# Kernel tuning notes

Measured on AMD Instinct MI355X. Metric: run time of the kernel, lower is better.

## Reference

```python
import jax, jax.numpy as jnp
import numpy as np

H = 8          # num heads
LN_EPS = 1e-5  # torch LayerNorm default

_SHAPES = {
    'src': (1024, 8, 256), 'pos': (1024, 8, 256), 'query_embed': (80, 8, 256), 'cam_mask': (8, 80, 1024),
    'enc_qkv_w': (2, 768, 256), 'enc_qkv_b': (2, 768), 'enc_out_w': (2, 256, 256), 'enc_out_b': (2, 256),
    'enc_ln1_g': (2, 256), 'enc_ln1_b': (2, 256),
    'enc_ff1_w': (2, 2048, 256), 'enc_ff1_b': (2, 2048), 'enc_ff2_w': (2, 256, 2048), 'enc_ff2_b': (2, 256),
    'enc_ln2_g': (2, 256), 'enc_ln2_b': (2, 256),
    'dec_sa_qkv_w': (2, 768, 256), 'dec_sa_qkv_b': (2, 768), 'dec_sa_out_w': (2, 256, 256), 'dec_sa_out_b': (2, 256),
    'dec_ln1_g': (2, 256), 'dec_ln1_b': (2, 256),
    'dec_ca_qkv_w': (2, 768, 256), 'dec_ca_qkv_b': (2, 768), 'dec_ca_out_w': (2, 256, 256), 'dec_ca_out_b': (2, 256),
    'dec_ln2_g': (2, 256), 'dec_ln2_b': (2, 256),
    'dec_ff1_w': (2, 2048, 256), 'dec_ff1_b': (2, 2048), 'dec_ff2_w': (2, 256, 2048), 'dec_ff2_b': (2, 256),
    'dec_ln3_g': (2, 256), 'dec_ln3_b': (2, 256),
    'dec_norm_g': (256,), 'dec_norm_b': (256,),
}


def setup_inputs() -> dict:
    key = jax.random.key(0)
    out = {}
    for i, (name, sh) in enumerate(_SHAPES.items()):
        k = jax.random.fold_in(key, i)
        if name.endswith('_g'):
            out[name] = jnp.ones(sh, jnp.float32)
        elif name.endswith('ln1_b') or name.endswith('ln2_b') or name.endswith('ln3_b') or name == 'dec_norm_b':
            out[name] = jnp.zeros(sh, jnp.float32)
        else:
            scale = 1.0 if name in ('src', 'pos', 'query_embed', 'cam_mask') else 0.02
            out[name] = jax.random.normal(k, sh, dtype=jnp.float32) * scale
    return out


def layer_norm(x, g, b):
    mu = jnp.mean(x, axis=-1, keepdims=True)
    var = jnp.mean(jnp.square(x - mu), axis=-1, keepdims=True)
    return (x - mu) * jax.lax.rsqrt(var + LN_EPS) * g + b


def mha(q_in, k_in, v_in, qkv_w, qkv_b, out_w, out_b, bias=None):
    # q_in: [L,B,D], k_in/v_in: [S,B,D]; torch layout: projections are x @ W.T + b
    L, B, D = q_in.shape
    S = k_in.shape[0]
    hd = D // H
    wq, wk, wv = qkv_w[:D], qkv_w[D:2 * D], qkv_w[2 * D:]
    bq, bk, bv = qkv_b[:D], qkv_b[D:2 * D], qkv_b[2 * D:]
    q = (q_in @ wq.T + bq).reshape(L, B, H, hd).transpose(1, 2, 0, 3)  # [B,H,L,hd]
    k = (k_in @ wk.T + bk).reshape(S, B, H, hd).transpose(1, 2, 0, 3)  # [B,H,S,hd]
    v = (v_in @ wv.T + bv).reshape(S, B, H, hd).transpose(1, 2, 0, 3)
    logits = jnp.einsum('bhld,bhsd->bhls', q, k) * (1.0 / np.sqrt(hd))
    if bias is not None:
        logits = logits + bias[:, None, :, :]  # CAM bias broadcast over heads
    attn = jax.nn.softmax(logits, axis=-1)
    o = jnp.einsum('bhls,bhsd->bhld', attn, v).transpose(2, 0, 1, 3).reshape(L, B, D)
    return o @ out_w.T + out_b


def reference(src, pos, query_embed, cam_mask,
              enc_qkv_w, enc_qkv_b, enc_out_w, enc_out_b, enc_ln1_g, enc_ln1_b,
              enc_ff1_w, enc_ff1_b, enc_ff2_w, enc_ff2_b, enc_ln2_g, enc_ln2_b,
              dec_sa_qkv_w, dec_sa_qkv_b, dec_sa_out_w, dec_sa_out_b, dec_ln1_g, dec_ln1_b,
              dec_ca_qkv_w, dec_ca_qkv_b, dec_ca_out_w, dec_ca_out_b, dec_ln2_g, dec_ln2_b,
              dec_ff1_w, dec_ff1_b, dec_ff2_w, dec_ff2_b, dec_ln3_g, dec_ln3_b,
              dec_norm_g, dec_norm_b):
    n_enc = enc_qkv_w.shape[0]
    n_dec = dec_sa_qkv_w.shape[0]
    # --- encoder (post-norm DETR style, pos added to q,k) ---
    mem = src
    for i in range(n_enc):
        qk = mem + pos
        a = mha(qk, qk, mem, enc_qkv_w[i], enc_qkv_b[i], enc_out_w[i], enc_out_b[i])
        mem = layer_norm(mem + a, enc_ln1_g[i], enc_ln1_b[i])
        f = jax.nn.relu(mem @ enc_ff1_w[i].T + enc_ff1_b[i]) @ enc_ff2_w[i].T + enc_ff2_b[i]
        mem = layer_norm(mem + f, enc_ln2_g[i], enc_ln2_b[i])
    # --- decoder: tgt starts at zeros (Q2L), query_embed is query_pos ---
    tgt = jnp.zeros_like(query_embed)
    for i in range(n_dec):
        qk = tgt + query_embed
        sa = mha(qk, qk, tgt, dec_sa_qkv_w[i], dec_sa_qkv_b[i], dec_sa_out_w[i], dec_sa_out_b[i])
        tgt = layer_norm(tgt + sa, dec_ln1_g[i], dec_ln1_b[i])
        ca = mha(tgt + query_embed, mem + pos, mem,
                 dec_ca_qkv_w[i], dec_ca_qkv_b[i], dec_ca_out_w[i], dec_ca_out_b[i],
                 bias=cam_mask)  # MA: CAM-derived additive attention bias [B,L,S]
        tgt = layer_norm(tgt + ca, dec_ln2_g[i], dec_ln2_b[i])
        f = jax.nn.relu(tgt @ dec_ff1_w[i].T + dec_ff1_b[i]) @ dec_ff2_w[i].T + dec_ff2_b[i]
        tgt = layer_norm(tgt + f, dec_ln3_g[i], dec_ln3_b[i])
    out = layer_norm(tgt, dec_norm_g, dec_norm_b)
    return out[None]  # [1, L, B, D] as in TransformerDecoder's output.unsqueeze(0)
```

## Files before the change

kernel.cpp:

```cpp
#include <hip/hip_runtime.h>
#include <hip/hip_bf16.h>
#include <cstdint>
#include <cstddef>

typedef __hip_bfloat16 bf16;
typedef float f4 __attribute__((ext_vector_type(4)));
typedef float f32x4 __attribute__((ext_vector_type(4)));
typedef short s8v __attribute__((ext_vector_type(8)));
typedef unsigned short u16x4 __attribute__((ext_vector_type(4)));
typedef unsigned short u16x8 __attribute__((ext_vector_type(8)));

#define LN_EPS 1e-5f
#define LOG2E 1.4426950408889634f

#if __has_builtin(__builtin_amdgcn_exp2f)
__device__ __forceinline__ float EXP2(float x) { return __builtin_amdgcn_exp2f(x); }
#else
__device__ __forceinline__ float EXP2(float x) {
  float r; asm("v_exp_f32 %0, %1" : "=v"(r) : "v"(x)); return r;
}
#endif

__device__ __forceinline__ void async_cp16(const void* g, void* lds) {
  __builtin_amdgcn_global_load_lds(
      (const __attribute__((address_space(1))) unsigned int*)g,
      (__attribute__((address_space(3))) unsigned int*)lds, 16, 0, 0);
}

__device__ __forceinline__ uint32_t pkbf(float lo, float hi) {
#if __has_builtin(__builtin_amdgcn_perm)
  uint32_t l = __builtin_bit_cast(uint32_t, lo) + 0x8000u;
  uint32_t h = __builtin_bit_cast(uint32_t, hi) + 0x8000u;
  return __builtin_amdgcn_perm(h, l, 0x07060302u);
#else
  uint32_t l = __builtin_bit_cast(uint32_t, lo) + 0x8000u;
  uint32_t h = __builtin_bit_cast(uint32_t, hi) + 0x8000u;
  return (l >> 16) | (h & 0xFFFF0000u);
#endif
}

#define NCAST 17
struct CastArgs {
  const float* in[NCAST];
  bf16* out[NCAST];
  int end4[NCAST];
  int nseg;
};

__global__ __launch_bounds__(256) void cast_multi(CastArgs a, int total4) {
  int i = blockIdx.x * 256 + threadIdx.x;
  if (i >= total4) return;
  int s = 0;
  while (i >= a.end4[s]) ++s;
  int j = i - (s ? a.end4[s - 1] : 0);
  f4 v = ((const f4*)a.in[s])[j];
  u16x4 o;
#pragma unroll
  for (int c = 0; c < 4; ++c) {
    bf16 h = __float2bfloat16(v[c]);
    o[c] = *reinterpret_cast<unsigned short*>(&h);
  }
  ((u16x4*)a.out[s])[j] = o;
}

__global__ __launch_bounds__(256) void scale_f32_kernel(const float* __restrict__ in,
                                                        float* __restrict__ out,
                                                        float s, int n4) {
  int i = blockIdx.x * 256 + threadIdx.x;
  if (i < n4) {
    f4 v = ((const f4*)in)[i];
    ((f4*)out)[i] = v * s;
  }
}

__global__ __launch_bounds__(256) void add_bf16_kernel(const float* __restrict__ a,
                                                       const float* __restrict__ b,
                                                       bf16* __restrict__ out, int n4) {
  int i = blockIdx.x * 256 + threadIdx.x;
  if (i < n4) {
    f4 x = ((const f4*)a)[i];
    f4 y = ((const f4*)b)[i];
    u16x4 o;
#pragma unroll
    for (int j = 0; j < 4; ++j) {
      bf16 h = __float2bfloat16(x[j] + y[j]);
      o[j] = *reinterpret_cast<unsigned short*>(&h);
    }
    ((u16x4*)out)[i] = o;
  }
}

__global__ __launch_bounds__(256) void sa0_row(
    const float* __restrict__ Wo, const float* __restrict__ bv,
    const float* __restrict__ bo, const float* __restrict__ g,
    const float* __restrict__ b, float* __restrict__ row_out) {
  const int j = threadIdx.x;
  float acc = bo[j];
  for (int k = 0; k < 256; k += 4) {
    f4 w = *(const f4*)(Wo + (size_t)j * 256 + k);
    f4 v = *(const f4*)(bv + k);
    acc += w[0] * v[0] + w[1] * v[1] + w[2] * v[2] + w[3] * v[3];
  }
  float s = acc, s2 = acc * acc;
#pragma unroll
  for (int off = 32; off >= 1; off >>= 1) {
    s += __shfl_down(s, off);
    s2 += __shfl_down(s2, off);
  }
  __shared__ float red[8];
  int wv = j >> 6;
  if ((j & 63) == 0) { red[wv] = s; red[4 + wv] = s2; }
  __syncthreads();
  if (j == 0) {
    float ts = red[0] + red[1] + red[2] + red[3];
    float ts2 = red[4] + red[5] + red[6] + red[7];
    float mu = ts * (1.f / 256.f);
    float var = ts2 * (1.f / 256.f) - mu * mu;
    red[0] = mu;
    red[1] = rsqrtf(var + LN_EPS);
  }
  __syncthreads();
  row_out[j] = (acc - red[0]) * red[1] * g[j] + b[j];
}

__global__ __launch_bounds__(256) void sa0_bcast(
    const float* __restrict__ row, const float* __restrict__ qe,
    float* __restrict__ tgt, bf16* __restrict__ tgtb, bf16* __restrict__ tqkb) {
  const int r = blockIdx.x, j = threadIdx.x;
  float y = row[j];
  size_t idx = (size_t)r * 256 + j;
  tgt[idx] = y;
  tgtb[idx] = __float2bfloat16(y);
  tqkb[idx] = __float2bfloat16(y + qe[idx]);
}

template <int TB, int MODE, int SPLITK>
__global__ __launch_bounds__(256, 2) void mfma_gemm(
    const bf16* __restrict__ A, const bf16* __restrict__ W,
    const float* __restrict__ bias, float* __restrict__ C,
    bf16* __restrict__ Cb, int M, int N, int K, int HL, float qscale,
    const bf16* __restrict__ A2, bf16* __restrict__ Cb2, int nyA, int secV) {
  constexpr int WM = TB / 2, WN = TB / 2;
  constexpr int MR = WM / 16, NR = WN / 16;
  constexpr int NCH = TB / 32;
  __shared__ __attribute__((aligned(16))) unsigned short SH[TB * 128];
  unsigned short (*As)[64] = (unsigned short(*)[64])SH;
  unsigned short (*Ws)[64] = (unsigned short(*)[64])(SH + TB * 64);
  const int tid = threadIdx.x;
  const int lane = tid & 63, wave = tid >> 6;
  const int wr = wave >> 1, wc = wave & 1;
  const int bm = blockIdx.x * TB, bn = blockIdx.y * TB;
  const int fr = lane & 15, fo = lane >> 4;
  const int srowi = lane >> 3;
  const int slot = lane & 7;
  const int gcol = (slot ^ srowi) * 8;

  const bf16* Aeff = (MODE == 6) ? (((int)blockIdx.y < nyA) ? A : A2) : A;

  const int kchunk = K / SPLITK;
  const int kbeg = (SPLITK > 1) ? blockIdx.z * kchunk : 0;

  f32x4 acc[MR][NR] = {};

  for (int k0 = kbeg; k0 < kbeg + kchunk; k0 += 64) {
    __syncthreads();
#pragma unroll
    for (int c = 0; c < NCH; ++c) {
      int rbase = wave * (TB / 4) + c * 8;
      int row = rbase + srowi;
      async_cp16(Aeff + (size_t)(bm + row) * K + k0 + gcol, &As[rbase][0]);
      async_cp16(W + (size_t)(bn + row) * K + k0 + gcol, &Ws[rbase][0]);
    }
    __syncthreads();
#pragma unroll
    for (int ks = 0; ks < 2; ++ks) {
      s8v a[MR], b[NR];
#pragma unroll
      for (int mi = 0; mi < MR; ++mi) {
        int row = wr * WM + mi * 16 + fr;
        a[mi] = *(const s8v*)((const char*)&As[0][0] + row * 128 +
                              ((ks * 64 + fo * 16) ^ ((row & 7) << 4)));
      }
#pragma unroll
      for (int ni = 0; ni < NR; ++ni) {
        int row = wc * WN + ni * 16 + fr;
        b[ni] = *(const s8v*)((const char*)&Ws[0][0] + row * 128 +
                              ((ks * 64 + fo * 16) ^ ((row & 7) << 4)));
      }
#pragma unroll
      for (int mi = 0; mi < MR; ++mi)
#pragma unroll
        for (int ni = 0; ni < NR; ++ni)
          acc[mi][ni] = __builtin_amdgcn_mfma_f32_16x16x32_bf16(
              a[mi], b[ni], acc[mi][ni], 0, 0, 0);
    }
  }

  const int r0 = (lane >> 4) * 4;

  if (MODE == 5 || (MODE == 6 && (bn >> 8) >= secV)) {
    __syncthreads();
    unsigned short (*T)[72] = (unsigned short(*)[72])SH;
#pragma unroll
    for (int mi = 0; mi < MR; ++mi)
#pragma unroll
      for (int ni = 0; ni < NR; ++ni) {
        int colL = wc * WN + ni * 16 + fr;
        float bv = bias[bn + colL];
#pragma unroll
        for (int r = 0; r < 4; ++r) {
          int rowL = wr * WM + mi * 16 + r0 + r;
          bf16 hv = __float2bfloat16(acc[mi][ni][r] + bv);
          T[colL][rowL] = *(unsigned short*)&hv;
        }
      }
    __syncthreads();
    bf16* Cv = (MODE == 6) ? Cb2 : Cb;
    const int secBase = (MODE == 6) ? secV : 0;
    const int lbase = bm >> 3;
#pragma unroll
    for (int jj = 0; jj < 2; ++jj) {
      int cid = tid * 2 + jj;
      int colL = cid >> 3, bb = cid & 7;
      int c = bn + colL;
      int sec = (c >> 8) - secBase, hh = (c >> 5) & 7, d = c & 31;
      u16x8 v;
#pragma unroll
      for (int l = 0; l < 8; ++l) v[l] = T[colL][bb + 8 * l];
      *(u16x8*)(Cv + (size_t)sec * ((size_t)64 * 32 * HL) +
                ((size_t)(bb * 8 + hh) * 32 + d) * HL + lbase) = v;
    }
    return;
  }

  float* Cz = (MODE == 4) ? C + (size_t)blockIdx.z * M * N : C;
#pragma unroll
  for (int mi = 0; mi < MR; ++mi) {
#pragma unroll
    for (int ni = 0; ni < NR; ++ni) {
      int col = bn + wc * WN + ni * 16 + fr;
      float bv = (MODE == 4) ? 0.f : bias[col];
#pragma unroll
      for (int r = 0; r < 4; ++r) {
        int row = bm + wr * WM + mi * 16 + r0 + r;
        float t = acc[mi][ni][r] + bv;
        if (MODE == 2) t = fmaxf(t, 0.f);
        if (MODE == 0) {
          C[(size_t)row * N + col] = t;
        } else if (MODE == 4) {
          Cz[(size_t)row * N + col] = t;
        } else if (MODE == 3 || MODE == 6) {
          int l = row >> 3, bb = row & 7;
          int sec = col >> 8, hh = (col >> 5) & 7, d = col & 31;
          if (sec == 0) t *= qscale;
          Cb[(size_t)sec * ((size_t)64 * HL * 32) +
             ((size_t)(bb * 8 + hh) * HL + l) * 32 + d] = __float2bfloat16(t);
        } else {
          Cb[(size_t)row * N + col] = __float2bfloat16(t);
        }
      }
    }
  }
}

template <int HAS_BIAS, int PARTIAL, int NW>
__global__ __launch_bounds__(NW * 64, 3) void attn_mfma(
    const bf16* __restrict__ Qh, const bf16* __restrict__ Kh,
    const bf16* __restrict__ VhT, const float* __restrict__ bias,
    bf16* __restrict__ O, float* __restrict__ PO, float* __restrict__ PM,
    float* __restrict__ PL, int L, int S, int SC) {
  __shared__ __attribute__((aligned(16))) uint32_t Ps2[NW][2][16][36];
  const int tid = threadIdx.x;
  const int lane = tid & 63, wave = tid >> 6;
  const int fr = lane & 15, fo = lane >> 4;
  const int bh = blockIdx.x;
  const int b = bh >> 3, h = bh & 7;
  const int q0 = blockIdx.y * (NW * 16) + wave * 16;
  const int q = q0 + fr;

  const int cz = PARTIAL ? blockIdx.z : 0;
  const int sb = PARTIAL ? cz * SC : 0;
  const int se = PARTIAL ? min(S, sb + SC) : S;
  const int ng = (se - sb + 63) >> 6;

  s8v qf = {};
  if (q < L) qf = *(const s8v*)(Qh + ((size_t)bh * L + q) * 32 + fo * 8);

  const float* brow = nullptr;
  if (HAS_BIAS) brow = bias + ((size_t)b * L + (q < L ? q : L - 1)) * S;

  const bf16* Kbase = Kh + (size_t)bh * S * 32;
  const bf16* Vbase = VhT + (size_t)bh * 32 * S;

  float mA = -1e30f, lsA = 0.f, mB = -1e30f, lsB = 0.f;
  f32x4 oA[2] = {}, oB[2] = {};

  for (int g = 0; g < ng; g += 2) {
    const int sA = sb + g * 64, sB = sA + 64;

    s8v kA[4], kB[4], vA[2][2], vB[2][2];
#pragma unroll
    for (int kb = 0; kb < 4; ++kb) {
      kA[kb] = *(const s8v*)(Kbase + (size_t)(sA + kb * 16 + fr) * 32 + fo * 8);
      kB[kb] = *(const s8v*)(Kbase + (size_t)(sB + kb * 16 + fr) * 32 + fo * 8);
    }
#pragma unroll
    for (int dh = 0; dh < 2; ++dh)
#pragma unroll
      for (int ks = 0; ks < 2; ++ks) {
        vA[dh][ks] = *(const s8v*)(Vbase + (size_t)(dh * 16 + fr) * S +
                                   sA + ks * 32 + fo * 8);
        vB[dh][ks] = *(const s8v*)(Vbase + (size_t)(dh * 16 + fr) * S +
                                   sB + ks * 32 + fo * 8);
      }
    f4 bA[4], bB[4];
    if (HAS_BIAS) {
#pragma unroll
      for (int kb = 0; kb < 4; ++kb) {
        bA[kb] = *(const f4*)(brow + sA + kb * 16 + 4 * fo);
        bB[kb] = *(const f4*)(brow + sB + kb * 16 + 4 * fo);
      }
    }

    float lgA[16], lgB[16];
    __builtin_amdgcn_s_setprio(1);
#pragma unroll
    for (int kb = 0; kb < 4; ++kb) {
      f32x4 z = {};
      f32x4 sa = __builtin_amdgcn_mfma_f32_16x16x32_bf16(kA[kb], qf, z, 0, 0, 0);
#pragma unroll
      for (int r = 0; r < 4; ++r) lgA[kb * 4 + r] = sa[r];
    }
#pragma unroll
    for (int kb = 0; kb < 4; ++kb) {
      f32x4 z = {};
      f32x4 sa = __builtin_amdgcn_mfma_f32_16x16x32_bf16(kB[kb], qf, z, 0, 0, 0);
#pragma unroll
      for (int r = 0; r < 4; ++r) lgB[kb * 4 + r] = sa[r];
    }
    __builtin_amdgcn_s_setprio(0);
    if (HAS_BIAS) {
#pragma unroll
      for (int i = 0; i < 16; ++i) { lgA[i] += bA[i >> 2][i & 3]; lgB[i] += bB[i >> 2][i & 3]; }
    }
    if (sB + 64 > se) {
#pragma unroll
      for (int i = 0; i < 16; ++i) {
        int keyA = sA + (i >> 2) * 16 + 4 * fo + (i & 3);
        int keyB = sB + (i >> 2) * 16 + 4 * fo + (i & 3);
        if (keyA >= se) lgA[i] = -1e30f;
        if (keyB >= se) lgB[i] = -1e30f;
      }
    }

    float tA, tB;
    {
      float a0 = fmaxf(fmaxf(lgA[0], lgA[1]), fmaxf(lgA[2], lgA[3]));
      float a1 = fmaxf(fmaxf(lgA[4], lgA[5]), fmaxf(lgA[6], lgA[7]));
      float a2 = fmaxf(fmaxf(lgA[8], lgA[9]), fmaxf(lgA[10], lgA[11]));
      float a3 = fmaxf(fmaxf(lgA[12], lgA[13]), fmaxf(lgA[14], lgA[15]));
      tA = fmaxf(fmaxf(a0, a1), fmaxf(a2, a3));
      float b0 = fmaxf(fmaxf(lgB[0], lgB[1]), fmaxf(lgB[2], lgB[3]));
      float b1 = fmaxf(fmaxf(lgB[4], lgB[5]), fmaxf(lgB[6], lgB[7]));
      float b2 = fmaxf(fmaxf(lgB[8], lgB[9]), fmaxf(lgB[10], lgB[11]));
      float b3 = fmaxf(fmaxf(lgB[12], lgB[13]), fmaxf(lgB[14], lgB[15]));
      tB = fmaxf(fmaxf(b0, b1), fmaxf(b2, b3));
    }
    tA = fmaxf(tA, __shfl_xor(tA, 16));
    tB = fmaxf(tB, __shfl_xor(tB, 16));
    tA = fmaxf(tA, __shfl_xor(tA, 32));
    tB = fmaxf(tB, __shfl_xor(tB, 32));

    float nmA = fmaxf(mA, tA), nmB = fmaxf(mB, tB);
    float rsA = EXP2(mA - nmA), rsB = EXP2(mB - nmB);
    mA = nmA; mB = nmB;

    float psA = 0.f, psB = 0.f;
#pragma unroll
    for (int i = 0; i < 16; ++i) {
      lgA[i] = EXP2(lgA[i] - nmA); psA += lgA[i];
      lgB[i] = EXP2(lgB[i] - nmB); psB += lgB[i];
    }
    lsA = lsA * rsA + psA;
    lsB = lsB * rsB + psB;

#pragma unroll
    for (int kb = 0; kb < 4; ++kb) {
      uint32_t a0 = pkbf(lgA[kb * 4 + 0], lgA[kb * 4 + 1]);
      uint32_t a1 = pkbf(lgA[kb * 4 + 2], lgA[kb * 4 + 3]);
      *(uint64_t*)&Ps2[wave][0][fr][kb * 8 + 2 * fo] =
          (uint64_t)a0 | ((uint64_t)a1 << 32);
      uint32_t b0 = pkbf(lgB[kb * 4 + 0], lgB[kb * 4 + 1]);
      uint32_t b1 = pkbf(lgB[kb * 4 + 2], lgB[kb * 4 + 3]);
      *(uint64_t*)&Ps2[wave][1][fr][kb * 8 + 2 * fo] =
          (uint64_t)b0 | ((uint64_t)b1 << 32);
    }

#pragma unroll
    for (int r = 0; r < 4; ++r) {
      oA[0][r] *= rsA; oA[1][r] *= rsA;
      oB[0][r] *= rsB; oB[1][r] *= rsB;
    }
    s8v pA[2], pB[2];
#pragma unroll
    for (int ks = 0; ks < 2; ++ks) {
      pA[ks] = *(const s8v*)&Ps2[wave][0][fr][ks * 16 + 4 * fo];
      pB[ks] = *(const s8v*)&Ps2[wave][1][fr][ks * 16 + 4 * fo];
    }
    __builtin_amdgcn_s_setprio(1);
#pragma unroll
    for (int dh = 0; dh < 2; ++dh)
#pragma unroll
      for (int ks = 0; ks < 2; ++ks) {
        oA[dh] = __builtin_amdgcn_mfma_f32_16x16x32_bf16(vA[dh][ks], pA[ks], oA[dh], 0, 0, 0);
        oB[dh] = __builtin_amdgcn_mfma_f32_16x16x32_bf16(vB[dh][ks], pB[ks], oB[dh], 0, 0, 0);
      }
    __builtin_amdgcn_s_setprio(0);
  }

  float m = fmaxf(mA, mB);
  float wA = EXP2(mA - m), wB = EXP2(mB - m);
  float lsum = lsA * wA + lsB * wB;
  f32x4 oacc[2];
#pragma unroll
  for (int dh = 0; dh < 2; ++dh)
#pragma unroll
    for (int r = 0; r < 4; ++r)
      oacc[dh][r] = oA[dh][r] * wA + oB[dh][r] * wB;

  lsum += __shfl_xor(lsum, 16);
  lsum += __shfl_xor(lsum, 32);

  if (q < L) {
    if (PARTIAL) {
      size_t pi = ((size_t)cz * 64 + bh) * L + q;
      float* po = PO + pi * 32;
#pragma unroll
      for (int dh = 0; dh < 2; ++dh) {
        f4 t2;
#pragma unroll
        for (int r = 0; r < 4; ++r) t2[r] = oacc[dh][r];
        *(f4*)(po + dh * 16 + 4 * fo) = t2;
      }
      if (fo == 0) { PM[pi] = m; PL[pi] = lsum; }
    } else {
      float inv = 1.f / lsum;
      bf16* op = O + ((size_t)q * 8 + b) * 256 + h * 32;
#pragma unroll
      for (int dh = 0; dh < 2; ++dh) {
        uint32_t w0 = pkbf(oacc[dh][0] * inv, oacc[dh][1] * inv);
        uint32_t w1 = pkbf(oacc[dh][2] * inv, oacc[dh][3] * inv);
        *(uint32_t*)(op + dh * 16 + 4 * fo) = w0;
        *(uint32_t*)(op + dh * 16 + 4 * fo + 2) = w1;
      }
    }
  }
}

__global__ __launch_bounds__(256) void attn_combine(
    const float* __restrict__ PO, const float* __restrict__ PM,
    const float* __restrict__ PL, bf16* __restrict__ O, int L, int NC) {
  int gid = blockIdx.x * 256 + threadIdx.x;
  if (gid >= 64 * L * 32) return;
  int d = gid & 31;
  int rem = gid >> 5;
  int q = rem % L, bh = rem / L;
  int b = bh >> 3, h = bh & 7;
  float M = -1e30f;
  for (int c = 0; c < NC; ++c) M = fmaxf(M, PM[((size_t)c * 64 + bh) * L + q]);
  float lsum = 0.f, o = 0.f;
  for (int c = 0; c < NC; ++c) {
    size_t pi = ((size_t)c * 64 + bh) * L + q;
    float w = EXP2(PM[pi] - M);
    lsum += PL[pi] * w;
    o += PO[pi * 32 + d] * w;
  }
  O[((size_t)q * 8 + b) * 256 + h * 32 + d] = __float2bfloat16(o / lsum);
}

__global__ __launch_bounds__(256) void ln_kernel(
    const float* __restrict__ x, const float* __restrict__ res,
    const float* __restrict__ parts, int nparts, int pstride,
    const float* __restrict__ gbias,
    const float* __restrict__ g, const float* __restrict__ b,
    float* __restrict__ out, bf16* __restrict__ outb,
    const float* __restrict__ aux, bf16* __restrict__ auxb) {
  const int row = blockIdx.x, tid = threadIdx.x;
  size_t idx = (size_t)row * 256 + tid;
  float v = x[idx];
  if (res) v += res[idx];
  if (parts) {
    for (int z = 0; z < nparts; ++z) v += parts[(size_t)z * pstride + idx];
  }
  if (gbias) v += gbias[tid];
  float s = v, s2 = v * v;
#pragma unroll
  for (int off = 32; off >= 1; off >>= 1) {
    s += __shfl_down(s, off);
    s2 += __shfl_down(s2, off);
  }
  __shared__ float red[8];
  int wv = tid >> 6;
  if ((tid & 63) == 0) { red[wv] = s; red[4 + wv] = s2; }
  __syncthreads();
  if (tid == 0) {
    float ts = red[0] + red[1] + red[2] + red[3];
    float ts2 = red[4] + red[5] + red[6] + red[7];
    float mu = ts * (1.f / 256.f);
    float var = ts2 * (1.f / 256.f) - mu * mu;
    red[0] = mu;
    red[1] = rsqrtf(var + LN_EPS);
  }
  __syncthreads();
  float y = (v - red[0]) * red[1] * g[tid] + b[tid];
  if (out) out[idx] = y;
  if (outb) outb[idx] = __float2bfloat16(y);
  if (auxb) auxb[idx] = __float2bfloat16(y + aux[idx]);
}

extern "C" void kernel_launch(void* const* d_in, const int* in_sizes, int n_in,
                              void* d_out, int out_size, void* d_ws, size_t ws_size,
                              hipStream_t stream) {
  const float* src         = (const float*)d_in[0];
  const float* pos         = (const float*)d_in[1];
  const float* query_embed = (const float*)d_in[2];
  const float* cam_mask    = (const float*)d_in[3];
  const float* enc_qkv_w   = (const float*)d_in[4];
  const float* enc_qkv_b   = (const float*)d_in[5];
  const float* enc_out_w   = (const float*)d_in[6];
  const float* enc_out_b   = (const float*)d_in[7];
  const float* enc_ln1_g   = (const float*)d_in[8];
  const float* enc_ln1_b   = (const float*)d_in[9];
  const float* enc_ff1_w   = (const float*)d_in[10];
  const float* enc_ff1_b   = (const float*)d_in[11];
  const float* enc_ff2_w   = (const float*)d_in[12];
  const float* enc_ff2_b   = (const float*)d_in[13];
  const float* enc_ln2_g   = (const float*)d_in[14];
  const float* enc_ln2_b   = (const float*)d_in[15];
  const float* dec_sa_qkv_w= (const float*)d_in[16];
  const float* dec_sa_qkv_b= (const float*)d_in[17];
  const float* dec_sa_out_w= (const float*)d_in[18];
  const float* dec_sa_out_b= (const float*)d_in[19];
  const float* dec_ln1_g   = (const float*)d_in[20];
  const float* dec_ln1_b   = (const float*)d_in[21];
  const float* dec_ca_qkv_w= (const float*)d_in[22];
  const float* dec_ca_qkv_b= (const float*)d_in[23];
  const float* dec_ca_out_w= (const float*)d_in[24];
  const float* dec_ca_out_b= (const float*)d_in[25];
  const float* dec_ln2_g   = (const float*)d_in[26];
  const float* dec_ln2_b   = (const float*)d_in[27];
  const float* dec_ff1_w   = (const float*)d_in[28];
  const float* dec_ff1_b   = (const float*)d_in[29];
  const float* dec_ff2_w   = (const float*)d_in[30];
  const float* dec_ff2_b   = (const float*)d_in[31];
  const float* dec_ln3_g   = (const float*)d_in[32];
  const float* dec_ln3_b   = (const float*)d_in[33];
  const float* dec_norm_g  = (const float*)d_in[34];
  const float* dec_norm_b  = (const float*)d_in[35];

  size_t off = 0;
  char* base = (char*)d_ws;
  auto af = [&](size_t n) { float* p = (float*)(base + off); off += n * 4; return p; };
  auto ab = [&](size_t n) { bf16*  p = (bf16*)(base + off);  off += n * 2; return p; };

  float* mem  = af(2097152);
  float* PO   = af(8388608);
  float* pm   = af(262144);
  float* pl   = af(262144);
  float* cmlog= af(655360);
  float* pb   = af(1024);
  float* row0 = af(256);
  float* tgt  = af(163840);
  bf16* memb  = ab(2097152);
  bf16* qkb   = ab(2097152);
  bf16* aob   = ab(2097152);
  bf16* ffb   = ab(16777216);
  bf16* bufQ  = ab(4194304);
  bf16* bufK  = ab(4194304);
  bf16* bufV  = ab(4194304);
  bf16* bufVsa= ab(172032);
  bf16* tgtb  = ab(163840);
  bf16* tqkb  = ab(163840);
  bf16* taob  = ab(163840);
  bf16* qeb   = ab(163840);
  bf16* tffb  = ab(1310720);
  bf16* w_enc_qkv = ab(393216);
  bf16* w_enc_out = ab(131072);
  bf16* w_enc_ff1 = ab(1048576);
  bf16* w_enc_ff2 = ab(1048576);
  bf16* w_sa_qkv  = ab(393216);
  bf16* w_sa_out  = ab(131072);
  bf16* w_ca_q    = ab(131072);
  bf16* w_ca_kv   = ab(262144);
  bf16* w_ca_out  = ab(131072);
  bf16* w_dec_ff1 = ab(1048576);
  bf16* w_dec_ff2 = ab(1048576);

  const float qscale = 0.17677669529663687f * LOG2E;

  {
    CastArgs ca;
    const float* ins[NCAST] = {
        enc_qkv_w, enc_out_w, enc_ff1_w, enc_ff2_w,
        dec_sa_qkv_w, dec_sa_out_w,
        dec_ca_qkv_w,
        dec_ca_qkv_w + 65536,
        dec_ca_qkv_w + 131072,
        dec_ca_qkv_w + 196608,
        dec_ca_qkv_w + 262144,
        dec_ca_qkv_w + 327680,
        dec_ca_out_w, dec_ff1_w, dec_ff2_w, src, query_embed};
    bf16* outs[NCAST] = {
        w_enc_qkv, w_enc_out, w_enc_ff1, w_enc_ff2,
        w_sa_qkv, w_sa_out,
        w_ca_q,
        w_ca_kv,
        w_ca_kv + 131072,
        w_ca_q + 65536,
        w_ca_kv + 65536,
        w_ca_kv + 196608,
        w_ca_out, w_dec_ff1, w_dec_ff2, memb, qeb};
    int n4s[NCAST] = {98304, 32768, 262144, 262144, 98304, 32768,
                      16384, 16384, 16384, 16384, 16384, 16384,
                      32768, 262144, 262144, 524288, 40960};
    int acc = 0;
    for (int s = 0; s < NCAST; ++s) {
      ca.in[s] = ins[s]; ca.out[s] = outs[s];
      acc += n4s[s]; ca.end4[s] = acc;
    }
    ca.nseg = NCAST;
    cast_multi<<<(acc + 255) / 256, 256, 0, stream>>>(ca, acc);
  }
  scale_f32_kernel<<<640, 256, 0, stream>>>(cam_mask, cmlog, LOG2E, 163840);
  hipMemcpyAsync(mem, src, (size_t)2097152 * 4, hipMemcpyDeviceToDevice, stream);
  hipMemcpyAsync(pb,       dec_ca_qkv_b + 256,       1024, hipMemcpyDeviceToDevice, stream);
  hipMemcpyAsync(pb + 256, dec_ca_qkv_b + 768 + 256, 1024, hipMemcpyDeviceToDevice, stream);
  hipMemcpyAsync(pb + 512, dec_ca_qkv_b + 512,       1024, hipMemcpyDeviceToDevice, stream);
  hipMemcpyAsync(pb + 768, dec_ca_qkv_b + 768 + 512, 1024, hipMemcpyDeviceToDevice, stream);

  auto g64_head = [&](const bf16* A, const bf16* W, const float* bias, bf16* Cb,
                      int M, int N, int K, int HL, float qs) {
    mfma_gemm<64, 3, 1><<<dim3(M / 64, N / 64), 256, 0, stream>>>(
        A, W, bias, nullptr, Cb, M, N, K, HL, qs, nullptr, nullptr, 0, 0);
  };
  auto g64_relu = [&](const bf16* A, const bf16* W, const float* bias, bf16* Cb,
                      int M, int N, int K) {
    mfma_gemm<64, 2, 1><<<dim3(M / 64, N / 64), 256, 0, stream>>>(
        A, W, bias, nullptr, Cb, M, N, K, 0, 1.f, nullptr, nullptr, 0, 0);
  };
  auto g128_relu = [&](const bf16* A, const bf16* W, const float* bias, bf16* Cb,
                       int M, int N, int K) {
    mfma_gemm<128, 2, 1><<<dim3(M / 128, N / 128), 256, 0, stream>>>(
        A, W, bias, nullptr, Cb, M, N, K, 0, 1.f, nullptr, nullptr, 0, 0);
  };

  add_bf16_kernel<<<2048, 256, 0, stream>>>(mem, pos, qkb, 524288);
  for (int i = 0; i < 2; ++i) {
    const bf16* wq = w_enc_qkv + (size_t)i * 196608;
    const float* qkvb = enc_qkv_b + (size_t)i * 768;
    mfma_gemm<64, 6, 1><<<dim3(128, 12), 256, 0, stream>>>(
        qkb, wq, qkvb, nullptr, bufQ, 8192, 768, 256, 1024, qscale,
        memb, bufV, 8, 2);
    attn_mfma<0, 0, 4><<<dim3(64, 16), 256, 0, stream>>>(
        bufQ, bufQ + 2097152, bufV, nullptr, aob, nullptr, nullptr, nullptr,
        1024, 1024, 0);
    mfma_gemm<64, 4, 2><<<dim3(128, 4, 2), 256, 0, stream>>>(
        aob, w_enc_out + (size_t)i * 65536, nullptr, PO, nullptr,
        8192, 256, 256, 0, 1.f, nullptr, nullptr, 0, 0);
    ln_kernel<<<8192, 256, 0, stream>>>(mem, nullptr, PO, 2, 2097152,
                                        enc_out_b + i * 256,
                                        enc_ln1_g + i * 256, enc_ln1_b + i * 256,
                                        mem, memb, nullptr, nullptr);
    g128_relu(memb, w_enc_ff1 + (size_t)i * 524288, enc_ff1_b + i * 2048, ffb,
              8192, 2048, 256);
    mfma_gemm<64, 4, 2><<<dim3(128, 4, 2), 256, 0, stream>>>(
        ffb, w_enc_ff2 + (size_t)i * 524288, nullptr, PO, nullptr,
        8192, 256, 2048, 0, 1.f, nullptr, nullptr, 0, 0);
    ln_kernel<<<8192, 256, 0, stream>>>(mem, nullptr, PO, 2, 2097152,
                                        enc_ff2_b + i * 256,
                                        enc_ln2_g + i * 256, enc_ln2_b + i * 256,
                                        mem, memb, pos, qkb);
  }

  mfma_gemm<64, 6, 1><<<dim3(128, 16), 256, 0, stream>>>(
      qkb, w_ca_kv, pb, nullptr, bufK, 8192, 1024, 256, 1024, 1.f,
      memb, bufV, 8, 2);

  for (int i = 0; i < 2; ++i) {
    const float* sab = dec_sa_qkv_b + (size_t)i * 768;
    const float* cab = dec_ca_qkv_b + (size_t)i * 768;

    if (i == 0) {
      sa0_row<<<1, 256, 0, stream>>>(dec_sa_out_w, dec_sa_qkv_b + 512,
                                     dec_sa_out_b, dec_ln1_g, dec_ln1_b, row0);
      sa0_bcast<<<640, 256, 0, stream>>>(row0, query_embed, tgt, tgtb, tqkb);
    } else {
      const bf16* wsa = w_sa_qkv + (size_t)i * 196608;
      mfma_gemm<64, 6, 1><<<dim3(10, 12), 256, 0, stream>>>(
          tqkb, wsa, sab, nullptr, bufQ, 640, 768, 256, 80, qscale,
          tgtb, bufVsa, 8, 2);
      attn_mfma<0, 0, 1><<<dim3(64, 5), 64, 0, stream>>>(
          bufQ, bufQ + 163840, bufVsa, nullptr, taob, nullptr, nullptr, nullptr,
          80, 80, 0);
      mfma_gemm<64, 4, 4><<<dim3(10, 4, 4), 256, 0, stream>>>(
          taob, w_sa_out + (size_t)i * 65536, nullptr, PO, nullptr,
          640, 256, 256, 0, 1.f, nullptr, nullptr, 0, 0);
      ln_kernel<<<640, 256, 0, stream>>>(tgt, nullptr, PO, 4, 163840,
                                         dec_sa_out_b + i * 256,
                                         dec_ln1_g + i * 256, dec_ln1_b + i * 256,
                                         tgt, tgtb, query_embed, tqkb);
    }
    g64_head(tqkb, w_ca_q + (size_t)i * 65536, cab, bufQ, 640, 256, 256, 80, qscale);
    attn_mfma<1, 1, 1><<<dim3(64, 5, 8), 64, 0, stream>>>(
        bufQ, bufK + (size_t)i * 2097152, bufV + (size_t)i * 2097152, cmlog,
        nullptr, PO + 4194304, pm, pl, 80, 1024, 128);
    attn_combine<<<640, 256, 0, stream>>>(PO + 4194304, pm, pl, taob, 80, 8);
    mfma_gemm<64, 4, 4><<<dim3(10, 4, 4), 256, 0, stream>>>(
        taob, w_ca_out + (size_t)i * 65536, nullptr, PO, nullptr,
        640, 256, 256, 0, 1.f, nullptr, nullptr, 0, 0);
    ln_kernel<<<640, 256, 0, stream>>>(tgt, nullptr, PO, 4, 163840,
                                       dec_ca_out_b + i * 256,
                                       dec_ln2_g + i * 256, dec_ln2_b + i * 256,
                                       tgt, tgtb, nullptr, nullptr);
    g64_relu(tgtb, w_dec_ff1 + (size_t)i * 524288, dec_ff1_b + i * 2048, tffb,
             640, 2048, 256);
    mfma_gemm<64, 4, 4><<<dim3(10, 4, 4), 256, 0, stream>>>(
        tffb, w_dec_ff2 + (size_t)i * 524288, nullptr, PO, nullptr,
        640, 256, 2048, 0, 1.f, nullptr, nullptr, 0, 0);
    ln_kernel<<<640, 256, 0, stream>>>(tgt, nullptr, PO, 4, 163840,
                                       dec_ff2_b + i * 256,
                                       dec_ln3_g + i * 256, dec_ln3_b + i * 256,
                                       tgt, tgtb, query_embed, tqkb);
  }

  ln_kernel<<<640, 256, 0, stream>>>(tgt, nullptr, nullptr, 0, 0, nullptr,
                                     dec_norm_g, dec_norm_b,
                                     (float*)d_out, nullptr, nullptr, nullptr);
}
```

Measured before the change: 396.8 us.

## Fuse prologue kernels, fold mask log2e scaling into attention, halve split-K

Replaces the separate src cast, the src copy into mem, and the src+pos add with one enc_prolog kernel. The first encoder LayerNorm now reads src directly. The four bias memcpys become a single pack_pb launch. The cam_mask pre-scaling kernel is removed, and the log2e factor is applied with an fma inside the attention kernel. The cross-attention key split drops from 8 chunks of 128 to 4 chunks of 256, which cuts launches and combine work but exposes less parallelism.

```diff
diff --git a/kernel.cpp b/kernel.cpp
--- a/kernel.cpp
+++ b/kernel.cpp
@@ -39,7 +39,7 @@
 #endif
 }
 
-#define NCAST 17
+#define NCAST 16
 struct CastArgs {
   const float* in[NCAST];
   bf16* out[NCAST];
@@ -63,31 +63,33 @@
   ((u16x4*)a.out[s])[j] = o;
 }
 
-__global__ __launch_bounds__(256) void scale_f32_kernel(const float* __restrict__ in,
-                                                        float* __restrict__ out,
-                                                        float s, int n4) {
+__global__ __launch_bounds__(256) void enc_prolog(
+    const float* __restrict__ src, const float* __restrict__ pos,
+    bf16* __restrict__ memb, bf16* __restrict__ qkb, int n4) {
   int i = blockIdx.x * 256 + threadIdx.x;
   if (i < n4) {
-    f4 v = ((const f4*)in)[i];
-    ((f4*)out)[i] = v * s;
-  }
-}
-
-__global__ __launch_bounds__(256) void add_bf16_kernel(const float* __restrict__ a,
-                                                       const float* __restrict__ b,
-                                                       bf16* __restrict__ out, int n4) {
-  int i = blockIdx.x * 256 + threadIdx.x;
-  if (i < n4) {
-    f4 x = ((const f4*)a)[i];
-    f4 y = ((const f4*)b)[i];
-    u16x4 o;
+    f4 s = ((const f4*)src)[i];
+    f4 p = ((const f4*)pos)[i];
+    u16x4 om, oq;
 #pragma unroll
     for (int j = 0; j < 4; ++j) {
-      bf16 h = __float2bfloat16(x[j] + y[j]);
-      o[j] = *reinterpret_cast<unsigned short*>(&h);
-    }
-    ((u16x4*)out)[i] = o;
-  }
+      bf16 hm = __float2bfloat16(s[j]);
+      bf16 hq = __float2bfloat16(s[j] + p[j]);
+      om[j] = *reinterpret_cast<unsigned short*>(&hm);
+      oq[j] = *reinterpret_cast<unsigned short*>(&hq);
+    }
+    ((u16x4*)memb)[i] = om;
+    ((u16x4*)qkb)[i] = oq;
+  }
+}
+
+__global__ __launch_bounds__(256) void pack_pb(const float* __restrict__ qkvb,
+                                               float* __restrict__ pb) {
+  int j = threadIdx.x;
+  pb[j]       = qkvb[256 + j];
+  pb[256 + j] = qkvb[768 + 256 + j];
+  pb[512 + j] = qkvb[512 + j];
+  pb[768 + j] = qkvb[768 + 512 + j];
 }
 
 __global__ __launch_bounds__(256) void sa0_row(
@@ -341,7 +343,10 @@
     __builtin_amdgcn_s_setprio(0);
     if (HAS_BIAS) {
 #pragma unroll
-      for (int i = 0; i < 16; ++i) { lgA[i] += bA[i >> 2][i & 3]; lgB[i] += bB[i >> 2][i & 3]; }
+      for (int i = 0; i < 16; ++i) {
+        lgA[i] = fmaf(bA[i >> 2][i & 3], LOG2E, lgA[i]);
+        lgB[i] = fmaf(bB[i >> 2][i & 3], LOG2E, lgB[i]);
+      }
     }
     if (sB + 64 > se) {
 #pragma unroll
@@ -567,7 +572,6 @@
   float* PO   = af(8388608);
   float* pm   = af(262144);
   float* pl   = af(262144);
-  float* cmlog= af(655360);
   float* pb   = af(1024);
   float* row0 = af(256);
   float* tgt  = af(163840);
@@ -609,7 +613,7 @@
         dec_ca_qkv_w + 196608,
         dec_ca_qkv_w + 262144,
         dec_ca_qkv_w + 327680,
-        dec_ca_out_w, dec_ff1_w, dec_ff2_w, src, query_embed};
+        dec_ca_out_w, dec_ff1_w, dec_ff2_w, query_embed};
     bf16* outs[NCAST] = {
         w_enc_qkv, w_enc_out, w_enc_ff1, w_enc_ff2,
         w_sa_qkv, w_sa_out,
@@ -619,10 +623,10 @@
         w_ca_q + 65536,
         w_ca_kv + 65536,
         w_ca_kv + 196608,
-        w_ca_out, w_dec_ff1, w_dec_ff2, memb, qeb};
+        w_ca_out, w_dec_ff1, w_dec_ff2, qeb};
     int n4s[NCAST] = {98304, 32768, 262144, 262144, 98304, 32768,
                       16384, 16384, 16384, 16384, 16384, 16384,
-                      32768, 262144, 262144, 524288, 40960};
+                      32768, 262144, 262144, 40960};
     int acc = 0;
     for (int s = 0; s < NCAST; ++s) {
       ca.in[s] = ins[s]; ca.out[s] = outs[s];
@@ -631,12 +635,8 @@
     ca.nseg = NCAST;
     cast_multi<<<(acc + 255) / 256, 256, 0, stream>>>(ca, acc);
   }
-  scale_f32_kernel<<<640, 256, 0, stream>>>(cam_mask, cmlog, LOG2E, 163840);
-  hipMemcpyAsync(mem, src, (size_t)2097152 * 4, hipMemcpyDeviceToDevice, stream);
-  hipMemcpyAsync(pb,       dec_ca_qkv_b + 256,       1024, hipMemcpyDeviceToDevice, stream);
-  hipMemcpyAsync(pb + 256, dec_ca_qkv_b + 768 + 256, 1024, hipMemcpyDeviceToDevice, stream);
-  hipMemcpyAsync(pb + 512, dec_ca_qkv_b + 512,       1024, hipMemcpyDeviceToDevice, stream);
-  hipMemcpyAsync(pb + 768, dec_ca_qkv_b + 768 + 512, 1024, hipMemcpyDeviceToDevice, stream);
+  enc_prolog<<<2048, 256, 0, stream>>>(src, pos, memb, qkb, 524288);
+  pack_pb<<<1, 256, 0, stream>>>(dec_ca_qkv_b, pb);
 
   auto g64_head = [&](const bf16* A, const bf16* W, const float* bias, bf16* Cb,
                       int M, int N, int K, int HL, float qs) {
@@ -654,7 +654,6 @@
         A, W, bias, nullptr, Cb, M, N, K, 0, 1.f, nullptr, nullptr, 0, 0);
   };
 
-  add_bf16_kernel<<<2048, 256, 0, stream>>>(mem, pos, qkb, 524288);
   for (int i = 0; i < 2; ++i) {
     const bf16* wq = w_enc_qkv + (size_t)i * 196608;
     const float* qkvb = enc_qkv_b + (size_t)i * 768;
@@ -667,7 +666,7 @@
     mfma_gemm<64, 4, 2><<<dim3(128, 4, 2), 256, 0, stream>>>(
         aob, w_enc_out + (size_t)i * 65536, nullptr, PO, nullptr,
         8192, 256, 256, 0, 1.f, nullptr, nullptr, 0, 0);
-    ln_kernel<<<8192, 256, 0, stream>>>(mem, nullptr, PO, 2, 2097152,
+    ln_kernel<<<8192, 256, 0, stream>>>((i == 0) ? src : mem, nullptr, PO, 2, 2097152,
                                         enc_out_b + i * 256,
                                         enc_ln1_g + i * 256, enc_ln1_b + i * 256,
                                         mem, memb, nullptr, nullptr);
@@ -711,10 +710,10 @@
                                          tgt, tgtb, query_embed, tqkb);
     }
     g64_head(tqkb, w_ca_q + (size_t)i * 65536, cab, bufQ, 640, 256, 256, 80, qscale);
-    attn_mfma<1, 1, 1><<<dim3(64, 5, 8), 64, 0, stream>>>(
-        bufQ, bufK + (size_t)i * 2097152, bufV + (size_t)i * 2097152, cmlog,
-        nullptr, PO + 4194304, pm, pl, 80, 1024, 128);
-    attn_combine<<<640, 256, 0, stream>>>(PO + 4194304, pm, pl, taob, 80, 8);
+    attn_mfma<1, 1, 1><<<dim3(64, 5, 4), 64, 0, stream>>>(
+        bufQ, bufK + (size_t)i * 2097152, bufV + (size_t)i * 2097152, cam_mask,
+        nullptr, PO + 4194304, pm, pl, 80, 1024, 256);
+    attn_combine<<<640, 256, 0, stream>>>(PO + 4194304, pm, pl, taob, 80, 4);
     mfma_gemm<64, 4, 4><<<dim3(10, 4, 4), 256, 0, stream>>>(
         taob, w_ca_out + (size_t)i * 65536, nullptr, PO, nullptr,
         640, 256, 256, 0, 1.f, nullptr, nullptr, 0, 0);
```

Result: faster. 377.1 us, median of 2 (-5.0%).
